# Optimization experiments

Hardware: AMD Instinct MI355X
Metric: run time of the kernel (lower is better)

Reference implementation:

```python
import jax, jax.numpy as jnp
import numpy as np

EMBED_DIM = 1024
NUM_HEADS = 16
HEAD_DIM = EMBED_DIM // NUM_HEADS
FF_DIM = 4096
B, T = 4, 1024


def setup_inputs() -> dict:
    key = jax.random.key(0)
    ks = jax.random.split(key, 13)
    E, F = EMBED_DIM, FF_DIM
    s_e = 1.0 / np.sqrt(E)
    s_f = 1.0 / np.sqrt(F)
    return {
        "x": jax.random.normal(ks[0], (B, T, E), dtype=jnp.float32),
        "ln1_w": jnp.ones((E,), jnp.float32),
        "ln1_b": jnp.zeros((E,), jnp.float32),
        "ln2_w": jnp.ones((E,), jnp.float32),
        "ln2_b": jnp.zeros((E,), jnp.float32),
        "qkv_w": jax.random.uniform(ks[1], (3 * E, E), jnp.float32, -s_e, s_e),
        "qkv_b": jax.random.uniform(ks[2], (3 * E,), jnp.float32, -s_e, s_e),
        "out_w": jax.random.uniform(ks[3], (E, E), jnp.float32, -s_e, s_e),
        "out_b": jax.random.uniform(ks[4], (E,), jnp.float32, -s_e, s_e),
        "fc1_w": jax.random.uniform(ks[5], (F, E), jnp.float32, -s_e, s_e),
        "fc1_b": jax.random.uniform(ks[6], (F,), jnp.float32, -s_e, s_e),
        "fc2_w": jax.random.uniform(ks[7], (E, F), jnp.float32, -s_f, s_f),
        "fc2_b": jax.random.uniform(ks[8], (E,), jnp.float32, -s_f, s_f),
    }


def _layer_norm(x, w, b, eps=1e-5):
    mu = jnp.mean(x, axis=-1, keepdims=True)
    var = jnp.mean(jnp.square(x - mu), axis=-1, keepdims=True)
    return (x - mu) * jax.lax.rsqrt(var + eps) * w + b


def reference(x, ln1_w, ln1_b, ln2_w, ln2_b, qkv_w, qkv_b, out_w, out_b,
              fc1_w, fc1_b, fc2_w, fc2_b):
    Bn, Tn, C = x.shape
    H, D = NUM_HEADS, HEAD_DIM

    # --- causal self-attention (pre-LN) ---
    h = _layer_norm(x, ln1_w, ln1_b)
    qkv = h @ qkv_w.T + qkv_b  # [B,T,3E]
    qkv = qkv.reshape(Bn, Tn, 3, H, D).transpose(2, 0, 3, 1, 4)  # [3,B,H,T,D]
    q, k, v = qkv[0], qkv[1], qkv[2]
    scores = jnp.einsum("bhtd,bhsd->bhts", q, k) / np.sqrt(D).astype(np.float32)
    causal = jnp.tril(jnp.ones((Tn, Tn), dtype=bool))
    scores = jnp.where(causal, scores, -jnp.inf)
    probs = jax.nn.softmax(scores, axis=-1)  # dropout is identity at eval
    attn = jnp.einsum("bhts,bhsd->bhtd", probs, v)
    attn = attn.transpose(0, 2, 1, 3).reshape(Bn, Tn, C)
    attn = attn @ out_w.T + out_b
    x = x + attn

    # --- GELU MLP (pre-LN) ---
    h = _layer_norm(x, ln2_w, ln2_b)
    h = jax.nn.gelu(h @ fc1_w.T + fc1_b, approximate=False)
    h = h @ fc2_w.T + fc2_b
    return x + h
```

## Files before the change

kernel.cpp:

```cpp
#include <hip/hip_runtime.h>

typedef float floatx4 __attribute__((ext_vector_type(4)));
typedef short shortx8 __attribute__((ext_vector_type(8)));

#define E_DIM 1024
#define F_DIM 4096
#define BATCH 4
#define SEQ 1024
#define NH 16
#define HD 64
#define MROWS (BATCH*SEQ)
#define QKV_N (3*E_DIM)

typedef const __attribute__((address_space(1))) unsigned int* gas_ptr;
typedef __attribute__((address_space(3))) unsigned int* las_ptr;

__device__ __forceinline__ unsigned short f2bf(float f) {
    union { float f; unsigned u; } un; un.f = f;
    unsigned u = un.u;
    u += 0x7fffu + ((u >> 16) & 1u);
    return (unsigned short)(u >> 16);
}

__device__ __forceinline__ float gelu_fast(float v) {
    float u = 0.7978845608f * (v + 0.044715f * v * v * v);
    float t = __builtin_exp2f(-2.885390082f * u);
    return v * __builtin_amdgcn_rcpf(1.0f + t);
}

__device__ __forceinline__ void xcd_remap(int& m_idx, int& n_idx) {
    int nt = gridDim.x;
    int mt_x = gridDim.y >> 3;
    int lin = blockIdx.y * nt + blockIdx.x;
    int xcd = lin & 7, loc = lin >> 3;
    int n = loc / mt_x;
    int m_local = loc - n * mt_x;
    m_idx = xcd * mt_x + m_local;
    n_idx = n;
}

#define S_QKV (3*E_DIM*E_DIM)
#define S_WO  (E_DIM*E_DIM)
#define S_W1  (F_DIM*E_DIM)
#define S_TOT (S_QKV + S_WO + 2*S_W1)
__global__ __launch_bounds__(256) void f2b_all(
        const float* __restrict__ qkv_w, const float* __restrict__ out_w,
        const float* __restrict__ fc1_w, const float* __restrict__ fc2_w,
        unsigned short* __restrict__ wq, unsigned short* __restrict__ wo,
        unsigned short* __restrict__ w1, unsigned short* __restrict__ w2) {
    long idx = ((long)blockIdx.x * 256 + threadIdx.x) * 4;
    const float* src; unsigned short* dst; long off;
    if (idx < S_QKV)                    { src = qkv_w; dst = wq; off = idx; }
    else if (idx < S_QKV + S_WO)        { src = out_w; dst = wo; off = idx - S_QKV; }
    else if (idx < S_QKV + S_WO + S_W1) { src = fc1_w; dst = w1; off = idx - S_QKV - S_WO; }
    else                                { src = fc2_w; dst = w2; off = idx - S_QKV - S_WO - S_W1; }
    float4 v = *(const float4*)&src[off];
    ushort4 o;
    o.x = f2bf(v.x); o.y = f2bf(v.y); o.z = f2bf(v.z); o.w = f2bf(v.w);
    *(ushort4*)&dst[off] = o;
}

__global__ __launch_bounds__(256) void ln_kernel(const float* __restrict__ x,
                                                 const float* __restrict__ w,
                                                 const float* __restrict__ b,
                                                 unsigned short* __restrict__ out) {
    int row = blockIdx.x;
    const float* xr = x + (size_t)row * E_DIM;
    float v[4];
    float s = 0.f, ss = 0.f;
    for (int i = 0; i < 4; ++i) {
        v[i] = xr[threadIdx.x + i * 256];
        s += v[i]; ss += v[i] * v[i];
    }
    for (int m = 32; m; m >>= 1) { s += __shfl_xor(s, m); ss += __shfl_xor(ss, m); }
    __shared__ float red[8];
    int wave = threadIdx.x >> 6;
    if ((threadIdx.x & 63) == 0) { red[wave] = s; red[wave + 4] = ss; }
    __syncthreads();
    s = red[0] + red[1] + red[2] + red[3];
    ss = red[4] + red[5] + red[6] + red[7];
    float mu = s * (1.0f / E_DIM);
    float var = ss * (1.0f / E_DIM) - mu * mu;
    float rs = rsqrtf(var + 1e-5f);
    for (int i = 0; i < 4; ++i) {
        int c = threadIdx.x + i * 256;
        out[(size_t)row * E_DIM + c] = f2bf((v[i] - mu) * rs * w[c] + b[c]);
    }
}

#define BK 64

template<int EPI>
__global__ __launch_bounds__(1024) void gemm_16w(
        const unsigned short* __restrict__ A, const unsigned short* __restrict__ Bw,
        const float* __restrict__ bias, const float* __restrict__ resid,
        float* __restrict__ Cf, unsigned short* __restrict__ Cb,
        int M, int N, int K) {
    __shared__ unsigned short sA[2][256 * BK];
    __shared__ unsigned short sB[2][256 * BK];
    int tid = threadIdx.x;
    int wave = tid >> 6, lane = tid & 63;
    int m_idx, n_idx; xcd_remap(m_idx, n_idx);
    int m0 = m_idx * 256, n0 = n_idx * 256;
    int wm = (wave >> 2) * 64, wn = (wave & 3) * 64;
    int l15 = lane & 15, quad = lane >> 4;

    int srow = tid >> 3;
    int scg  = (tid & 7) ^ (srow & 7);
    const unsigned short* Ag = A  + (size_t)(m0 + srow) * K + scg * 8;
    const unsigned short* Bg = Bw + (size_t)(n0 + srow) * K + scg * 8;

    floatx4 acc[4][4];
#pragma unroll
    for (int i = 0; i < 4; ++i)
#pragma unroll
        for (int j = 0; j < 4; ++j) acc[i][j] = (floatx4)0.f;

    auto stage = [&](int kt, int bsel) {
        int k0 = kt * BK;
#pragma unroll
        for (int p = 0; p < 2; ++p) {
            __builtin_amdgcn_global_load_lds((gas_ptr)(Ag + k0 + (size_t)p * 128 * K),
                (las_ptr)&sA[bsel][(p * 128 + wave * 8) * BK], 16, 0, 0);
            __builtin_amdgcn_global_load_lds((gas_ptr)(Bg + k0 + (size_t)p * 128 * K),
                (las_ptr)&sB[bsel][(p * 128 + wave * 8) * BK], 16, 0, 0);
        }
    };

    int T = K / BK;
    stage(0, 0);
    stage(1, 1);
    for (int i = 0; i < T; ++i) {
        if (i + 1 < T) { asm volatile("s_waitcnt vmcnt(4)" ::: "memory"); }
        else           { asm volatile("s_waitcnt vmcnt(0)" ::: "memory"); }
        __builtin_amdgcn_s_barrier();
        int bs = i & 1;
#pragma unroll
        for (int kk8 = 0; kk8 < 8; kk8 += 4) {
            shortx8 af[4], bfr[4];
#pragma unroll
            for (int ii = 0; ii < 4; ++ii) {
                int R = wm + ii * 16 + l15;
                int sc = (quad + kk8) ^ (R & 7);
                af[ii] = *(const shortx8*)&sA[bs][(R * 8 + sc) * 8];
            }
#pragma unroll
            for (int j = 0; j < 4; ++j) {
                int R = wn + j * 16 + l15;
                int sc = (quad + kk8) ^ (R & 7);
                bfr[j] = *(const shortx8*)&sB[bs][(R * 8 + sc) * 8];
            }
#pragma unroll
            for (int ii = 0; ii < 4; ++ii)
#pragma unroll
                for (int j = 0; j < 4; ++j)
                    acc[ii][j] = __builtin_amdgcn_mfma_f32_16x16x32_bf16(af[ii], bfr[j], acc[ii][j], 0, 0, 0);
        }
        __builtin_amdgcn_s_barrier();
        if (i + 2 < T) stage(i + 2, bs);
    }

#pragma unroll
    for (int i = 0; i < 4; ++i) {
        int row = m0 + wm + i * 16 + quad * 4;
#pragma unroll
        for (int j = 0; j < 4; ++j) {
            int col = n0 + wn + j * 16 + l15;
            float bs2 = bias[col];
#pragma unroll
            for (int r = 0; r < 4; ++r) {
                float v = acc[i][j][r] + bs2;
                int rr = row + r;
                if (EPI & 1) v = gelu_fast(v);
                if (EPI & 2) v += resid[(size_t)rr * N + col];
                if (EPI & 4) Cf[(size_t)rr * N + col] = v;
                if (EPI & 8) Cb[(size_t)rr * N + col] = f2bf(v);
            }
        }
    }
}

template<int EPI>
__global__ __launch_bounds__(1024) void gemm_ksp(
        const unsigned short* __restrict__ A, const unsigned short* __restrict__ Bw,
        const float* __restrict__ bias, const float* __restrict__ resid,
        float* __restrict__ Cf, unsigned short* __restrict__ Cb,
        int M, int N, int K) {
    __shared__ unsigned short smem[2][2][128 * 128];
    int tid = threadIdx.x;
    int wave = tid >> 6, lane = tid & 63;
    int m_idx, n_idx; xcd_remap(m_idx, n_idx);
    int m0 = m_idx * 128, n0 = n_idx * 128;
    int kq = wave & 3, mi = (wave >> 2) & 1, ni = wave >> 3;
    int l15 = lane & 15, quad = lane >> 4;
    int kh = kq >> 1, cb = (kq & 1) * 4;

    int lu = wave * 8 + (lane >> 3);

    floatx4 acc[4][4];
#pragma unroll
    for (int i = 0; i < 4; ++i)
#pragma unroll
        for (int j = 0; j < 4; ++j) acc[i][j] = (floatx4)0.f;

    auto stage = [&](int kt, int b) {
#pragma unroll
        for (int p = 0; p < 2; ++p) {
            int u = p * 128 + lu;
            int row = u >> 1, uh = u & 1;
            int scg = (lane & 7) ^ (row & 7);
            __builtin_amdgcn_global_load_lds(
                (gas_ptr)(A + (size_t)(m0 + row) * K + kt * 128 + uh * 64 + scg * 8),
                (las_ptr)&smem[b][0][(p * 128 + wave * 8) * 64], 16, 0, 0);
        }
#pragma unroll
        for (int p = 0; p < 2; ++p) {
            int u = p * 128 + lu;
            int row = u >> 1, uh = u & 1;
            int scg = (lane & 7) ^ (row & 7);
            __builtin_amdgcn_global_load_lds(
                (gas_ptr)(Bw + (size_t)(n0 + row) * K + kt * 128 + uh * 64 + scg * 8),
                (las_ptr)&smem[b][1][(p * 128 + wave * 8) * 64], 16, 0, 0);
        }
    };

    int T = K / 128;
    stage(0, 0);
    stage(1, 1);
    for (int i = 0; i < T; ++i) {
        if (i + 1 < T) { asm volatile("s_waitcnt vmcnt(4)" ::: "memory"); }
        else           { asm volatile("s_waitcnt vmcnt(0)" ::: "memory"); }
        __builtin_amdgcn_s_barrier();
        int bs = i & 1;
        shortx8 af[4], bfr[4];
#pragma unroll
        for (int ii = 0; ii < 4; ++ii) {
            int R = mi * 64 + ii * 16 + l15;
            int sc = (cb + quad) ^ (R & 7);
            af[ii] = *(const shortx8*)&smem[bs][0][((R * 2 + kh) * 8 + sc) * 8];
        }
#pragma unroll
        for (int j = 0; j < 4; ++j) {
            int R = ni * 64 + j * 16 + l15;
            int sc = (cb + quad) ^ (R & 7);
            bfr[j] = *(const shortx8*)&smem[bs][1][((R * 2 + kh) * 8 + sc) * 8];
        }
#pragma unroll
        for (int ii = 0; ii < 4; ++ii)
#pragma unroll
            for (int j = 0; j < 4; ++j)
                acc[ii][j] = __builtin_amdgcn_mfma_f32_16x16x32_bf16(af[ii], bfr[j], acc[ii][j], 0, 0, 0);
        __builtin_amdgcn_s_barrier();
        if (i + 2 < T) stage(i + 2, bs);
    }

    float* red = (float*)&smem[0][0][0];
    int base = (mi * 2 + ni) * 2;
    auto wracc = [&](int rid) {
#pragma unroll
        for (int i2 = 0; i2 < 4; ++i2)
#pragma unroll
            for (int j2 = 0; j2 < 4; ++j2)
                *(floatx4*)&red[(size_t)rid * 4096 + ((i2 * 4 + j2) * 64 + lane) * 4] = acc[i2][j2];
    };
    auto rdacc = [&](int rid) {
#pragma unroll
        for (int i2 = 0; i2 < 4; ++i2)
#pragma unroll
            for (int j2 = 0; j2 < 4; ++j2) {
                floatx4 v = *(const floatx4*)&red[(size_t)rid * 4096 + ((i2 * 4 + j2) * 64 + lane) * 4];
                acc[i2][j2] += v;
            }
    };
    if (kq >= 2) wracc(base + (kq - 2));
    __syncthreads();
    if (kq < 2) rdacc(base + kq);
    __syncthreads();
    if (kq == 1) wracc(base);
    __syncthreads();
    if (kq == 0) {
        rdacc(base);
#pragma unroll
        for (int i = 0; i < 4; ++i) {
            int row = m0 + mi * 64 + i * 16 + quad * 4;
#pragma unroll
            for (int j = 0; j < 4; ++j) {
                int col = n0 + ni * 64 + j * 16 + l15;
                float bs2 = bias[col];
#pragma unroll
                for (int r = 0; r < 4; ++r) {
                    float v = acc[i][j][r] + bs2;
                    int rr = row + r;
                    if (EPI & 1) v = gelu_fast(v);
                    if (EPI & 2) v += resid[(size_t)rr * N + col];
                    if (EPI & 4) Cf[(size_t)rr * N + col] = v;
                    if (EPI & 8) Cb[(size_t)rr * N + col] = f2bf(v);
                }
            }
        }
    }
}

__global__ __launch_bounds__(256) void vtrans_kernel(const unsigned short* __restrict__ qkv,
                                                     unsigned short* __restrict__ vT) {
    __shared__ unsigned short tile[64 * 72];
    int tid = threadIdx.x;
    int bh = blockIdx.y, b = bh >> 4, h = bh & 15;
    int t0 = blockIdx.x * 64;
    const unsigned short* vsrc = qkv + (size_t)b * SEQ * QKV_N + 2 * E_DIM + h * HD;
#pragma unroll
    for (int p = 0; p < 2; ++p) {
        int idx = p * 256 + tid;
        int row = idx >> 3, col = (idx & 7) * 8;
        *(shortx8*)&tile[row * 72 + col] =
            *(const shortx8*)&vsrc[(size_t)(t0 + row) * QKV_N + col];
    }
    __syncthreads();
    int d = tid >> 2, tch = (tid & 3) * 16;
    unsigned short* dst = vT + (size_t)bh * HD * SEQ + (size_t)d * SEQ + t0 + tch;
    shortx8 a0, a1;
#pragma unroll
    for (int j = 0; j < 8; ++j) a0[j] = (short)tile[(tch + j) * 72 + d];
#pragma unroll
    for (int j = 0; j < 8; ++j) a1[j] = (short)tile[(tch + 8 + j) * 72 + d];
    *(shortx8*)&dst[0] = a0;
    *(shortx8*)&dst[8] = a1;
}

__global__ __launch_bounds__(512) void attn_kernel(
        const unsigned short* __restrict__ qkv, const unsigned short* __restrict__ vT,
        unsigned short* __restrict__ out) {
    __shared__ unsigned short kt[2][64 * 64];
    __shared__ unsigned short vt[2][64 * 64];
    __shared__ unsigned short ps[8][16 * 64];
    int tid = threadIdx.x;
    int wave = tid >> 6, lane = tid & 63, l15 = lane & 15, quad = lane >> 4;
    int bh = blockIdx.y, b = bh >> 4, h = bh & 15;
    const unsigned short* qbase = qkv + (size_t)b * SEQ * QKV_N + h * HD;
    const unsigned short* kbase = qbase + E_DIM;
    const unsigned short* vtb = vT + (size_t)bh * HD * SEQ;

    int srl = lane >> 3;
    int scg = (lane & 7) ^ srl;
    const float scale = 0.125f * 1.44269504f;

    int grp = wave >> 2, wv = wave & 3;
    int qt = grp ? (15 - blockIdx.x) : blockIdx.x;
    int myntile = qt + 1;
    int ntile = 16 - blockIdx.x;
    int qrow = qt * 64 + wv * 16;

    auto stage = [&](int t, int bsel) {
        int s0 = t * 64;
        int rbase = wave * 8;
        __builtin_amdgcn_global_load_lds(
            (gas_ptr)&kbase[(size_t)(s0 + rbase + srl) * QKV_N + scg * 8],
            (las_ptr)&kt[bsel][rbase * 64], 16, 0, 0);
        __builtin_amdgcn_global_load_lds(
            (gas_ptr)&vtb[(size_t)(rbase + srl) * SEQ + s0 + scg * 8],
            (las_ptr)&vt[bsel][rbase * 64], 16, 0, 0);
    };

    shortx8 qa0 = *(const shortx8*)&qbase[(size_t)(qrow + l15) * QKV_N + quad * 8];
    shortx8 qa1 = *(const shortx8*)&qbase[(size_t)(qrow + l15) * QKV_N + 32 + quad * 8];

    floatx4 o[4];
    for (int d = 0; d < 4; ++d) o[d] = (floatx4)0.f;
    float mrun[4], lrun[4];
    for (int r = 0; r < 4; ++r) { mrun[r] = -1e30f; lrun[r] = 0.f; }

    stage(0, 0);
    for (int t = 0; t < ntile; ++t) {
        asm volatile("s_waitcnt vmcnt(0)" ::: "memory");
        __builtin_amdgcn_s_barrier();
        if (t + 1 < ntile) stage(t + 1, (t + 1) & 1);
        if (t < myntile) {
            int bsel = t & 1;
            int s0 = t * 64;

            floatx4 sfr[4];
#pragma unroll
            for (int ct = 0; ct < 4; ++ct) {
                int R = ct * 16 + l15;
                int sc0 = quad ^ (R & 7), sc1 = (4 + quad) ^ (R & 7);
                shortx8 kb0 = *(const shortx8*)&kt[bsel][(R * 8 + sc0) * 8];
                shortx8 kb1 = *(const shortx8*)&kt[bsel][(R * 8 + sc1) * 8];
                floatx4 s4 = (floatx4)0.f;
                s4 = __builtin_amdgcn_mfma_f32_16x16x32_bf16(qa0, kb0, s4, 0, 0, 0);
                s4 = __builtin_amdgcn_mfma_f32_16x16x32_bf16(qa1, kb1, s4, 0, 0, 0);
                sfr[ct] = s4;
            }

            bool masked = (t == myntile - 1);
#pragma unroll
            for (int r = 0; r < 4; ++r) {
                int qg = qrow + quad * 4 + r;
                float sv[4];
                float mx = mrun[r];
#pragma unroll
                for (int ct = 0; ct < 4; ++ct) {
                    float v = sfr[ct][r] * scale;
                    if (masked && (s0 + ct * 16 + l15 > qg)) v = -1e30f;
                    sv[ct] = v;
                    mx = fmaxf(mx, v);
                }
                for (int mm = 8; mm; mm >>= 1) mx = fmaxf(mx, __shfl_xor(mx, mm));
                float alpha = exp2f(mrun[r] - mx);
                mrun[r] = mx;
                float sum = 0.f;
                float pv[4];
#pragma unroll
                for (int ct = 0; ct < 4; ++ct) { pv[ct] = exp2f(sv[ct] - mx); sum += pv[ct]; }
                for (int mm = 8; mm; mm >>= 1) sum += __shfl_xor(sum, mm);
                lrun[r] = lrun[r] * alpha + sum;
#pragma unroll
                for (int d = 0; d < 4; ++d) o[d][r] *= alpha;
                int row = quad * 4 + r;
#pragma unroll
                for (int ct = 0; ct < 4; ++ct) {
                    int g = ct * 2 + (l15 >> 3);
                    int sc = g ^ (row & 7);
                    ps[wave][row * 64 + sc * 8 + (l15 & 7)] = f2bf(pv[ct]);
                }
            }
            shortx8 pa0, pa1;
            {
                int sc0 = quad ^ (l15 & 7), sc1 = (4 + quad) ^ (l15 & 7);
                pa0 = *(const shortx8*)&ps[wave][(l15 * 8 + sc0) * 8];
                pa1 = *(const shortx8*)&ps[wave][(l15 * 8 + sc1) * 8];
            }
#pragma unroll
            for (int d = 0; d < 4; ++d) {
                int R = d * 16 + l15;
                int sc0 = quad ^ (R & 7), sc1 = (4 + quad) ^ (R & 7);
                shortx8 vb0 = *(const shortx8*)&vt[bsel][(R * 8 + sc0) * 8];
                shortx8 vb1 = *(const shortx8*)&vt[bsel][(R * 8 + sc1) * 8];
                o[d] = __builtin_amdgcn_mfma_f32_16x16x32_bf16(pa0, vb0, o[d], 0, 0, 0);
                o[d] = __builtin_amdgcn_mfma_f32_16x16x32_bf16(pa1, vb1, o[d], 0, 0, 0);
            }
        }
    }

#pragma unroll
    for (int r = 0; r < 4; ++r) {
        float inv = 1.0f / lrun[r];
        int m = (b << 10) + qrow + quad * 4 + r;
#pragma unroll
        for (int d = 0; d < 4; ++d)
            out[(size_t)m * E_DIM + h * HD + d * 16 + l15] = f2bf(o[d][r] * inv);
    }
}

extern "C" void kernel_launch(void* const* d_in, const int* in_sizes, int n_in,
                              void* d_out, int out_size, void* d_ws, size_t ws_size,
                              hipStream_t stream) {
    const float* x     = (const float*)d_in[0];
    const float* ln1_w = (const float*)d_in[1];
    const float* ln1_b = (const float*)d_in[2];
    const float* ln2_w = (const float*)d_in[3];
    const float* ln2_b = (const float*)d_in[4];
    const float* qkv_w = (const float*)d_in[5];
    const float* qkv_b = (const float*)d_in[6];
    const float* out_w = (const float*)d_in[7];
    const float* out_b = (const float*)d_in[8];
    const float* fc1_w = (const float*)d_in[9];
    const float* fc1_b = (const float*)d_in[10];
    const float* fc2_w = (const float*)d_in[11];
    const float* fc2_b = (const float*)d_in[12];

    char* ws = (char*)d_ws;
    size_t off = 0;
    auto alloc = [&](size_t bytes) { char* p = ws + off; off += bytes; return p; };
    unsigned short* wq   = (unsigned short*)alloc((size_t)3 * E_DIM * E_DIM * 2);
    unsigned short* wo   = (unsigned short*)alloc((size_t)E_DIM * E_DIM * 2);
    unsigned short* w1   = (unsigned short*)alloc((size_t)F_DIM * E_DIM * 2);
    unsigned short* w2   = (unsigned short*)alloc((size_t)E_DIM * F_DIM * 2);
    unsigned short* h1   = (unsigned short*)alloc((size_t)MROWS * E_DIM * 2);
    unsigned short* qkvb = (unsigned short*)alloc((size_t)MROWS * QKV_N * 2);
    unsigned short* vT   = (unsigned short*)alloc((size_t)BATCH * NH * HD * SEQ * 2);
    unsigned short* attn = (unsigned short*)alloc((size_t)MROWS * E_DIM * 2);
    float*          x1   = (float*)alloc((size_t)MROWS * E_DIM * 4);
    unsigned short* h2   = (unsigned short*)alloc((size_t)MROWS * E_DIM * 2);
    unsigned short* g    = (unsigned short*)alloc((size_t)MROWS * F_DIM * 2);

    f2b_all<<<S_TOT / 4 / 256, 256, 0, stream>>>(qkv_w, out_w, fc1_w, fc2_w, wq, wo, w1, w2);

    ln_kernel<<<MROWS, 256, 0, stream>>>(x, ln1_w, ln1_b, h1);
    gemm_16w<8><<<dim3(QKV_N / 256, MROWS / 256), 1024, 0, stream>>>(
        h1, wq, qkv_b, nullptr, nullptr, qkvb, MROWS, QKV_N, E_DIM);
    vtrans_kernel<<<dim3(SEQ / 64, BATCH * NH), 256, 0, stream>>>(qkvb, vT);
    attn_kernel<<<dim3(8, BATCH * NH), 512, 0, stream>>>(qkvb, vT, attn);
    gemm_ksp<2 | 4><<<dim3(E_DIM / 128, MROWS / 128), 1024, 0, stream>>>(
        attn, wo, out_b, x, x1, nullptr, MROWS, E_DIM, E_DIM);
    ln_kernel<<<MROWS, 256, 0, stream>>>(x1, ln2_w, ln2_b, h2);
    gemm_16w<1 | 8><<<dim3(F_DIM / 256, MROWS / 256), 1024, 0, stream>>>(
        h2, w1, fc1_b, nullptr, nullptr, g, MROWS, F_DIM, E_DIM);
    gemm_ksp<2 | 4><<<dim3(E_DIM / 128, MROWS / 128), 1024, 0, stream>>>(
        g, w2, fc2_b, x1, (float*)d_out, nullptr, MROWS, E_DIM, F_DIM);
}
```

Baseline: 314.7 us.

## Load K and V fragments directly from global memory in attention kernel

Drops the shared-memory double-buffered K/V staging (global_load_lds plus per-tile barriers) and has each wave read its K and V^T MFMA operands straight from global memory. Each wave now loops only over its own causal tile count instead of the block-wide maximum, so waves no longer wait on each other at barriers. The cost is redundant global/L2 traffic, since all 8 waves fetch the same K/V tiles independently, and load latency is no longer hidden by prefetching.

Result: slower. 331.2 us (+5.3%).

```diff
diff --git a/kernel.cpp b/kernel.cpp
--- a/kernel.cpp
+++ b/kernel.cpp
@@ -330,8 +330,6 @@
 __global__ __launch_bounds__(512) void attn_kernel(
         const unsigned short* __restrict__ qkv, const unsigned short* __restrict__ vT,
         unsigned short* __restrict__ out) {
-    __shared__ unsigned short kt[2][64 * 64];
-    __shared__ unsigned short vt[2][64 * 64];
     __shared__ unsigned short ps[8][16 * 64];
     int tid = threadIdx.x;
     int wave = tid >> 6, lane = tid & 63, l15 = lane & 15, quad = lane >> 4;
@@ -339,27 +337,12 @@
     const unsigned short* qbase = qkv + (size_t)b * SEQ * QKV_N + h * HD;
     const unsigned short* kbase = qbase + E_DIM;
     const unsigned short* vtb = vT + (size_t)bh * HD * SEQ;
-
-    int srl = lane >> 3;
-    int scg = (lane & 7) ^ srl;
     const float scale = 0.125f * 1.44269504f;
 
     int grp = wave >> 2, wv = wave & 3;
     int qt = grp ? (15 - blockIdx.x) : blockIdx.x;
-    int myntile = qt + 1;
-    int ntile = 16 - blockIdx.x;
     int qrow = qt * 64 + wv * 16;
-
-    auto stage = [&](int t, int bsel) {
-        int s0 = t * 64;
-        int rbase = wave * 8;
-        __builtin_amdgcn_global_load_lds(
-            (gas_ptr)&kbase[(size_t)(s0 + rbase + srl) * QKV_N + scg * 8],
-            (las_ptr)&kt[bsel][rbase * 64], 16, 0, 0);
-        __builtin_amdgcn_global_load_lds(
-            (gas_ptr)&vtb[(size_t)(rbase + srl) * SEQ + s0 + scg * 8],
-            (las_ptr)&vt[bsel][rbase * 64], 16, 0, 0);
-    };
+    int ntile = qt + 1;
 
     shortx8 qa0 = *(const shortx8*)&qbase[(size_t)(qrow + l15) * QKV_N + quad * 8];
     shortx8 qa1 = *(const shortx8*)&qbase[(size_t)(qrow + l15) * QKV_N + 32 + quad * 8];
@@ -369,75 +352,66 @@
     float mrun[4], lrun[4];
     for (int r = 0; r < 4; ++r) { mrun[r] = -1e30f; lrun[r] = 0.f; }
 
-    stage(0, 0);
     for (int t = 0; t < ntile; ++t) {
-        asm volatile("s_waitcnt vmcnt(0)" ::: "memory");
-        __builtin_amdgcn_s_barrier();
-        if (t + 1 < ntile) stage(t + 1, (t + 1) & 1);
-        if (t < myntile) {
-            int bsel = t & 1;
-            int s0 = t * 64;
-
-            floatx4 sfr[4];
+        int s0 = t * 64;
+
+        floatx4 sfr[4];
+#pragma unroll
+        for (int ct = 0; ct < 4; ++ct) {
+            int R = s0 + ct * 16 + l15;
+            shortx8 kb0 = *(const shortx8*)&kbase[(size_t)R * QKV_N + quad * 8];
+            shortx8 kb1 = *(const shortx8*)&kbase[(size_t)R * QKV_N + 32 + quad * 8];
+            floatx4 s4 = (floatx4)0.f;
+            s4 = __builtin_amdgcn_mfma_f32_16x16x32_bf16(qa0, kb0, s4, 0, 0, 0);
+            s4 = __builtin_amdgcn_mfma_f32_16x16x32_bf16(qa1, kb1, s4, 0, 0, 0);
+            sfr[ct] = s4;
+        }
+
+        bool masked = (t == ntile - 1);
+#pragma unroll
+        for (int r = 0; r < 4; ++r) {
+            int qg = qrow + quad * 4 + r;
+            float sv[4];
+            float mx = mrun[r];
 #pragma unroll
             for (int ct = 0; ct < 4; ++ct) {
-                int R = ct * 16 + l15;
-                int sc0 = quad ^ (R & 7), sc1 = (4 + quad) ^ (R & 7);
-                shortx8 kb0 = *(const shortx8*)&kt[bsel][(R * 8 + sc0) * 8];
-                shortx8 kb1 = *(const shortx8*)&kt[bsel][(R * 8 + sc1) * 8];
-                floatx4 s4 = (floatx4)0.f;
-                s4 = __builtin_amdgcn_mfma_f32_16x16x32_bf16(qa0, kb0, s4, 0, 0, 0);
-                s4 = __builtin_amdgcn_mfma_f32_16x16x32_bf16(qa1, kb1, s4, 0, 0, 0);
-                sfr[ct] = s4;
-            }
-
-            bool masked = (t == myntile - 1);
-#pragma unroll
-            for (int r = 0; r < 4; ++r) {
-                int qg = qrow + quad * 4 + r;
-                float sv[4];
-                float mx = mrun[r];
-#pragma unroll
-                for (int ct = 0; ct < 4; ++ct) {
-                    float v = sfr[ct][r] * scale;
-                    if (masked && (s0 + ct * 16 + l15 > qg)) v = -1e30f;
-                    sv[ct] = v;
-                    mx = fmaxf(mx, v);
-                }
-                for (int mm = 8; mm; mm >>= 1) mx = fmaxf(mx, __shfl_xor(mx, mm));
-                float alpha = exp2f(mrun[r] - mx);
-                mrun[r] = mx;
-                float sum = 0.f;
-                float pv[4];
-#pragma unroll
-                for (int ct = 0; ct < 4; ++ct) { pv[ct] = exp2f(sv[ct] - mx); sum += pv[ct]; }
-                for (int mm = 8; mm; mm >>= 1) sum += __shfl_xor(sum, mm);
-                lrun[r] = lrun[r] * alpha + sum;
-#pragma unroll
-                for (int d = 0; d < 4; ++d) o[d][r] *= alpha;
-                int row = quad * 4 + r;
-#pragma unroll
-                for (int ct = 0; ct < 4; ++ct) {
-                    int g = ct * 2 + (l15 >> 3);
-                    int sc = g ^ (row & 7);
-                    ps[wave][row * 64 + sc * 8 + (l15 & 7)] = f2bf(pv[ct]);
-                }
-            }
-            shortx8 pa0, pa1;
-            {
-                int sc0 = quad ^ (l15 & 7), sc1 = (4 + quad) ^ (l15 & 7);
-                pa0 = *(const shortx8*)&ps[wave][(l15 * 8 + sc0) * 8];
-                pa1 = *(const shortx8*)&ps[wave][(l15 * 8 + sc1) * 8];
-            }
-#pragma unroll
-            for (int d = 0; d < 4; ++d) {
-                int R = d * 16 + l15;
-                int sc0 = quad ^ (R & 7), sc1 = (4 + quad) ^ (R & 7);
-                shortx8 vb0 = *(const shortx8*)&vt[bsel][(R * 8 + sc0) * 8];
-                shortx8 vb1 = *(const shortx8*)&vt[bsel][(R * 8 + sc1) * 8];
-                o[d] = __builtin_amdgcn_mfma_f32_16x16x32_bf16(pa0, vb0, o[d], 0, 0, 0);
-                o[d] = __builtin_amdgcn_mfma_f32_16x16x32_bf16(pa1, vb1, o[d], 0, 0, 0);
-            }
+                float v = sfr[ct][r] * scale;
+                if (masked && (s0 + ct * 16 + l15 > qg)) v = -1e30f;
+                sv[ct] = v;
+                mx = fmaxf(mx, v);
+            }
+            for (int mm = 8; mm; mm >>= 1) mx = fmaxf(mx, __shfl_xor(mx, mm));
+            float alpha = exp2f(mrun[r] - mx);
+            mrun[r] = mx;
+            float sum = 0.f;
+            float pv[4];
+#pragma unroll
+            for (int ct = 0; ct < 4; ++ct) { pv[ct] = exp2f(sv[ct] - mx); sum += pv[ct]; }
+            for (int mm = 8; mm; mm >>= 1) sum += __shfl_xor(sum, mm);
+            lrun[r] = lrun[r] * alpha + sum;
+#pragma unroll
+            for (int d = 0; d < 4; ++d) o[d][r] *= alpha;
+            int row = quad * 4 + r;
+#pragma unroll
+            for (int ct = 0; ct < 4; ++ct) {
+                int g = ct * 2 + (l15 >> 3);
+                int sc = g ^ (row & 7);
+                ps[wave][row * 64 + sc * 8 + (l15 & 7)] = f2bf(pv[ct]);
+            }
+        }
+        shortx8 pa0, pa1;
+        {
+            int sc0 = quad ^ (l15 & 7), sc1 = (4 + quad) ^ (l15 & 7);
+            pa0 = *(const shortx8*)&ps[wave][(l15 * 8 + sc0) * 8];
+            pa1 = *(const shortx8*)&ps[wave][(l15 * 8 + sc1) * 8];
+        }
+#pragma unroll
+        for (int d = 0; d < 4; ++d) {
+            int R = d * 16 + l15;
+            shortx8 vb0 = *(const shortx8*)&vtb[(size_t)R * SEQ + s0 + quad * 8];
+            shortx8 vb1 = *(const shortx8*)&vtb[(size_t)R * SEQ + s0 + 32 + quad * 8];
+            o[d] = __builtin_amdgcn_mfma_f32_16x16x32_bf16(pa0, vb0, o[d], 0, 0, 0);
+            o[d] = __builtin_amdgcn_mfma_f32_16x16x32_bf16(pa1, vb1, o[d], 0, 0, 0);
         }
     }
 
```
